# Optimization experiments

Measured on AMD Instinct MI355X. Metric: run time of the kernel, lower is better.

The kernel has to match this reference:

```python
import jax, jax.numpy as jnp
import numpy as np

B, S, D, H = 2, 2048, 1024, 16
DK = D // H
NEG = -1e9


def setup_inputs() -> dict:
    key = jax.random.key(0)
    ks = jax.random.split(key, 11)
    s = 1.0 / np.sqrt(D)
    inp = {
        "q": jax.random.normal(ks[0], (B, S, D), jnp.float32),
        "k": jax.random.normal(ks[1], (B, S, D), jnp.float32),
        "v": jax.random.normal(ks[2], (B, S, D), jnp.float32),
        "mask": jnp.tril(jnp.ones((S, S), jnp.int32))[None, None],  # [1,1,S,S] causal
        "Wq": jax.random.normal(ks[3], (D, D), jnp.float32) * s,
        "bq": jnp.zeros((D,), jnp.float32),
        "Wk": jax.random.normal(ks[4], (D, D), jnp.float32) * s,
        "bk": jnp.zeros((D,), jnp.float32),
        "Wv": jax.random.normal(ks[5], (D, D), jnp.float32) * s,
        "bv": jnp.zeros((D,), jnp.float32),
        "Wo": jax.random.normal(ks[6], (D, D), jnp.float32) * s,
        "bo": jnp.zeros((D,), jnp.float32),
    }
    return inp


def reference(q, k, v, mask, Wq, bq, Wk, bk, Wv, bv, Wo, bo):
    # projections (torch Linear: x @ W.T + b)
    Q = q @ Wq.T + bq
    K = k @ Wk.T + bk
    V = v @ Wv.T + bv
    # [B,S,D] -> [B,H,S,DK]
    Q = Q.reshape(B, S, H, DK).transpose(0, 2, 1, 3)
    K = K.reshape(B, S, H, DK).transpose(0, 2, 1, 3)
    V = V.reshape(B, S, H, DK).transpose(0, 2, 1, 3)
    scores = jnp.einsum("bhqd,bhkd->bhqk", Q, K) / jnp.sqrt(jnp.float32(DK))
    scores = jnp.where(mask == 0, jnp.float32(NEG), scores)
    attn = jax.nn.softmax(scores, axis=-1)  # dropout p=0.0 -> identity
    x = jnp.einsum("bhqk,bhkd->bhqd", attn, V)
    x = x.transpose(0, 2, 1, 3).reshape(B, S, D)
    return x @ Wo.T + bo
```

## Files before the change

kernel.cpp:

```cpp
#include <hip/hip_runtime.h>
#include <hip/hip_bf16.h>


typedef __bf16 bf16_t;
typedef __bf16 bf16x4 __attribute__((ext_vector_type(4)));
typedef __bf16 bf16x8 __attribute__((ext_vector_type(8)));
typedef float f32x4 __attribute__((ext_vector_type(4)));

#define BB 2
#define SS 2048
#define DD 1024
#define HH 16
#define DKK 64
#define MM 4096

#define NELT ((size_t)BB * SS * DD)
#define WELT ((size_t)DD * DD)

__device__ __align__(16) bf16_t g_ws[7 * NELT + 4 * WELT];

__device__ __forceinline__ void gld16(const bf16_t* g, bf16_t* l) {
    __builtin_amdgcn_global_load_lds(
        (const __attribute__((address_space(1))) void*)g,
        (__attribute__((address_space(3))) void*)l, 16, 0, 0);
}

__global__ __launch_bounds__(256) void cvt7(
    const float* __restrict__ q,  const float* __restrict__ k,  const float* __restrict__ v,
    const float* __restrict__ Wq, const float* __restrict__ Wk, const float* __restrict__ Wv,
    const float* __restrict__ Wo,
    bf16_t* __restrict__ qb, bf16_t* __restrict__ kb, bf16_t* __restrict__ vb,
    bf16_t* __restrict__ Wqb, bf16_t* __restrict__ Wkb, bf16_t* __restrict__ Wvb,
    bf16_t* __restrict__ Wob)
{
    const float* s; bf16_t* d; size_t n;
    switch (blockIdx.y) {
        case 0: s = q;  d = qb;  n = NELT; break;
        case 1: s = k;  d = kb;  n = NELT; break;
        case 2: s = v;  d = vb;  n = NELT; break;
        case 3: s = Wq; d = Wqb; n = WELT; break;
        case 4: s = Wk; d = Wkb; n = WELT; break;
        case 5: s = Wv; d = Wvb; n = WELT; break;
        default: s = Wo; d = Wob; n = WELT; break;
    }
    size_t e = ((size_t)blockIdx.x * 256 + threadIdx.x) * 8;
    if (e >= n) return;
    f32x4 a = *(const f32x4*)(s + e);
    f32x4 b = *(const f32x4*)(s + e + 4);
    bf16x8 o;
    #pragma unroll
    for (int i = 0; i < 4; ++i) { o[i] = (bf16_t)a[i]; o[4 + i] = (bf16_t)b[i]; }
    *(bf16x8*)(d + e) = o;
}

#define BM 128
#define BN 128
#define BKG 64
#define LDC 136

__global__ __launch_bounds__(256) void gemm_qkv3(
    const bf16_t* __restrict__ qb, const bf16_t* __restrict__ kb, const bf16_t* __restrict__ vb,
    const bf16_t* __restrict__ Wqb, const bf16_t* __restrict__ Wkb, const bf16_t* __restrict__ Wvb,
    const float* __restrict__ bq, const float* __restrict__ bk, const float* __restrict__ bv,
    bf16_t* __restrict__ Qp, bf16_t* __restrict__ Kp, bf16_t* __restrict__ Vt)
{
    const int z = blockIdx.z;
    const bf16_t* A    = (z == 0) ? qb  : (z == 1) ? kb  : vb;
    const bf16_t* W    = (z == 0) ? Wqb : (z == 1) ? Wkb : Wvb;
    const float*  bias = (z == 0) ? bq  : (z == 1) ? bk  : bv;

    __shared__ __align__(16) bf16_t smem[128 * LDC];
    bf16_t (*As)[BKG] = (bf16_t(*)[BKG])smem;
    bf16_t (*Bs)[BKG] = (bf16_t(*)[BKG])(smem + 128 * BKG);
    bf16_t (*Ct)[LDC] = (bf16_t(*)[LDC])smem;

    const int tid  = threadIdx.x;
    const int wave = tid >> 6;
    const int lane = tid & 63;
    const int quad = lane >> 4;
    const int c16  = lane & 15;
    const int bm = blockIdx.x * BM;
    const int bn = blockIdx.y * BN;
    const int wm = (wave >> 1) * 64;
    const int wn = (wave & 1) * 64;

    const int srow = lane >> 3;
    const int scol = (lane & 7) * 8;

    f32x4 acc[4][4] = {};

    for (int k0 = 0; k0 < DD; k0 += BKG) {
        __syncthreads();
        #pragma unroll
        for (int j = 0; j < 4; ++j) {
            int r0 = wave * 32 + j * 8;
            gld16(A + (size_t)(bm + r0 + srow) * DD + k0 + scol, &As[r0][0]);
            gld16(W + (size_t)(bn + r0 + srow) * DD + k0 + scol, &Bs[r0][0]);
        }
        __syncthreads();

        #pragma unroll
        for (int ks = 0; ks < 2; ++ks) {
            bf16x8 af[4], bfr[4];
            #pragma unroll
            for (int tm = 0; tm < 4; ++tm)
                af[tm] = *(const bf16x8*)(&As[wm + tm * 16 + c16][ks * 32 + quad * 8]);
            #pragma unroll
            for (int tn = 0; tn < 4; ++tn)
                bfr[tn] = *(const bf16x8*)(&Bs[wn + tn * 16 + c16][ks * 32 + quad * 8]);
            #pragma unroll
            for (int tm = 0; tm < 4; ++tm)
                #pragma unroll
                for (int tn = 0; tn < 4; ++tn)
                    acc[tm][tn] = __builtin_amdgcn_mfma_f32_16x16x32_bf16(
                        af[tm], bfr[tn], acc[tm][tn], 0, 0, 0);
        }
    }

    float bia[4];
    #pragma unroll
    for (int tn = 0; tn < 4; ++tn)
        bia[tn] = bias[bn + wn + tn * 16 + c16];

    if (z < 2) {
        const float osc = (z == 0) ? 0.125f : 1.0f;
        bf16_t* C = (z == 0) ? Qp : Kp;
        #pragma unroll
        for (int tm = 0; tm < 4; ++tm)
            #pragma unroll
            for (int r = 0; r < 4; ++r) {
                size_t base = (size_t)(bm + wm + tm * 16 + quad * 4 + r) * DD;
                #pragma unroll
                for (int tn = 0; tn < 4; ++tn)
                    C[base + bn + wn + tn * 16 + c16] =
                        (bf16_t)((acc[tm][tn][r] + bia[tn]) * osc);
            }
    } else {
        __syncthreads();
        #pragma unroll
        for (int tm = 0; tm < 4; ++tm)
            #pragma unroll
            for (int tn = 0; tn < 4; ++tn) {
                bf16x4 pk;
                #pragma unroll
                for (int r = 0; r < 4; ++r)
                    pk[r] = (bf16_t)(acc[tm][tn][r] + bia[tn]);
                *(bf16x4*)(&Ct[wn + tn * 16 + c16][wm + tm * 16 + quad * 4]) = pk;
            }
        __syncthreads();
        const int b_    = bm >> 11;
        const int sbase = bm & (SS - 1);
        #pragma unroll
        for (int p = 0; p < 4; ++p) {
            int col = p * 32 + (tid >> 3);
            int si  = (tid & 7) * 8;
            size_t rowoff = (size_t)(b_ * 1024 + bn + col) * SS + sbase;
            #pragma unroll
            for (int half = 0; half < 2; ++half) {
                int s = si + half * 64;
                *(bf16x8*)(&Vt[rowoff + s]) = *(const bf16x8*)(&Ct[col][s]);
            }
        }
    }
}

__global__ __launch_bounds__(256) void gemm_out(
    const bf16_t* __restrict__ A,
    const bf16_t* __restrict__ W,
    const float* __restrict__ bias,
    float* __restrict__ C)
{
    __shared__ __align__(16) bf16_t As[128][BKG];
    __shared__ __align__(16) bf16_t Bs[64][BKG];

    const int tid  = threadIdx.x;
    const int wave = tid >> 6;
    const int lane = tid & 63;
    const int quad = lane >> 4;
    const int c16  = lane & 15;
    const int bm = blockIdx.x * 128;
    const int bn = blockIdx.y * 64;
    const int wm = (wave >> 1) * 64;
    const int wn = (wave & 1) * 32;

    const int srow = lane >> 3;
    const int scol = (lane & 7) * 8;

    f32x4 acc[4][2] = {};

    for (int k0 = 0; k0 < DD; k0 += BKG) {
        __syncthreads();
        #pragma unroll
        for (int j = 0; j < 4; ++j) {
            int r0 = wave * 32 + j * 8;
            gld16(A + (size_t)(bm + r0 + srow) * DD + k0 + scol, &As[r0][0]);
        }
        #pragma unroll
        for (int j = 0; j < 2; ++j) {
            int r0 = wave * 16 + j * 8;
            gld16(W + (size_t)(bn + r0 + srow) * DD + k0 + scol, &Bs[r0][0]);
        }
        __syncthreads();

        #pragma unroll
        for (int ks = 0; ks < 2; ++ks) {
            bf16x8 af[4], bfr[2];
            #pragma unroll
            for (int tm = 0; tm < 4; ++tm)
                af[tm] = *(const bf16x8*)(&As[wm + tm * 16 + c16][ks * 32 + quad * 8]);
            #pragma unroll
            for (int tn = 0; tn < 2; ++tn)
                bfr[tn] = *(const bf16x8*)(&Bs[wn + tn * 16 + c16][ks * 32 + quad * 8]);
            #pragma unroll
            for (int tm = 0; tm < 4; ++tm)
                #pragma unroll
                for (int tn = 0; tn < 2; ++tn)
                    acc[tm][tn] = __builtin_amdgcn_mfma_f32_16x16x32_bf16(
                        af[tm], bfr[tn], acc[tm][tn], 0, 0, 0);
        }
    }

    float bia[2];
    #pragma unroll
    for (int tn = 0; tn < 2; ++tn)
        bia[tn] = bias[bn + wn + tn * 16 + c16];

    #pragma unroll
    for (int tm = 0; tm < 4; ++tm)
        #pragma unroll
        for (int r = 0; r < 4; ++r) {
            size_t base = (size_t)(bm + wm + tm * 16 + quad * 4 + r) * DD;
            #pragma unroll
            for (int tn = 0; tn < 2; ++tn)
                C[base + bn + wn + tn * 16 + c16] = acc[tm][tn][r] + bia[tn];
        }
}

#define LDPS 40
#define LDCF 68

__global__ __launch_bounds__(256) void attn_fwd7(
    const bf16_t* __restrict__ Q,
    const bf16_t* __restrict__ K,
    const bf16_t* __restrict__ Vt,
    bf16_t* __restrict__ O)
{
    const int flat = blockIdx.x;
    const int bh   = (flat & 7) * 4 + (flat >> 8);
    const int pair = (flat >> 3) & 31;
    const int b = bh >> 4;
    const int h = bh & 15;

    const int wave = threadIdx.x >> 6;
    const int lane = threadIdx.x & 63;
    const int quad = lane >> 4;
    const int c16  = lane & 15;

    __shared__ __align__(16) unsigned char smraw[4 * 16 * LDCF * 4];
    bf16_t (*Ps)[32][LDPS] = (bf16_t(*)[32][LDPS])smraw;
    float  (*Cf)[16][LDCF] = (float(*)[16][LDCF])smraw;
    __shared__ float Ls[4][32];

    const bf16_t* Kb = K  + (size_t)b * SS * DD + h * DKK;
    const bf16_t* Vb = Vt + (size_t)(b * 1024 + h * DKK) * SS;

    bf16_t*       pw = &Ps[wave][c16][quad * 4];
    const bf16_t* pr = &Ps[wave][c16][quad * 8];

    for (int t = 0; t < 2; ++t) {
        const int qt    = (t == 0) ? (63 - pair) : pair;
        const int qbase = qt * 32;
        const int U     = qt + 1;
        const int kend  = U * 32;

        bf16x8 qf[2][2];
        #pragma unroll
        for (int tm = 0; tm < 2; ++tm) {
            const bf16_t* qp = Q + ((size_t)b * SS + qbase + tm * 16 + c16) * DD + h * DKK;
            qf[tm][0] = *(const bf16x8*)(qp + quad * 8);
            qf[tm][1] = *(const bf16x8*)(qp + 32 + quad * 8);
        }

        f32x4 oacc[2][4] = {};
        float lsum2[2] = {0.f, 0.f};

        bf16x8 kfA[2][2], kfB[2][2];
        {
            int kb = wave * 32;
            #pragma unroll
            for (int ct = 0; ct < 2; ++ct) {
                const bf16_t* kp = Kb + (size_t)(kb + ct * 16 + c16) * DD;
                kfA[ct][0] = *(const bf16x8*)(kp + quad * 8);
                kfA[ct][1] = *(const bf16x8*)(kp + 32 + quad * 8);
            }
        }

        auto step = [&](int kb, bf16x8 (&kfc)[2][2], bf16x8 (&kfn)[2][2]) {
            f32x4 sc[2][2];
            #pragma unroll
            for (int tm = 0; tm < 2; ++tm)
                #pragma unroll
                for (int ct = 0; ct < 2; ++ct) {
                    f32x4 s = {};
                    s = __builtin_amdgcn_mfma_f32_16x16x32_bf16(kfc[ct][0], qf[tm][0], s, 0, 0, 0);
                    s = __builtin_amdgcn_mfma_f32_16x16x32_bf16(kfc[ct][1], qf[tm][1], s, 0, 0, 0);
                    sc[tm][ct] = s;
                }

            if (kb + 128 < kend) {
                #pragma unroll
                for (int ct = 0; ct < 2; ++ct) {
                    const bf16_t* kp = Kb + (size_t)(kb + 128 + ct * 16 + c16) * DD;
                    kfn[ct][0] = *(const bf16x8*)(kp + quad * 8);
                    kfn[ct][1] = *(const bf16x8*)(kp + 32 + quad * 8);
                }
            }

            bf16x8 vf[4];
            #pragma unroll
            for (int tn = 0; tn < 4; ++tn)
                vf[tn] = *(const bf16x8*)(Vb + (size_t)(tn * 16 + c16) * SS + kb + quad * 8);

            const bool needmask = (kb == qbase);
            #pragma unroll
            for (int tm = 0; tm < 2; ++tm) {
                const int qrow = qbase + tm * 16 + c16;
                #pragma unroll
                for (int ct = 0; ct < 2; ++ct) {
                    bf16x4 w;
                    #pragma unroll
                    for (int r = 0; r < 4; ++r) {
                        float s = sc[tm][ct][r];
                        if (needmask && (kb + ct * 16 + quad * 4 + r > qrow)) s = -1e9f;
                        float p = __expf(s);
                        lsum2[tm] += p;
                        w[r] = (bf16_t)p;
                    }
                    *(bf16x4*)(pw + tm * 16 * LDPS + ct * 16) = w;
                }
            }

            asm volatile("s_waitcnt lgkmcnt(0)" ::: "memory");

            #pragma unroll
            for (int tm = 0; tm < 2; ++tm) {
                bf16x8 pa = *(const bf16x8*)(pr + tm * 16 * LDPS);
                #pragma unroll
                for (int tn = 0; tn < 4; ++tn)
                    oacc[tm][tn] = __builtin_amdgcn_mfma_f32_16x16x32_bf16(
                        pa, vf[tn], oacc[tm][tn], 0, 0, 0);
            }
        };

        {
            int u = wave; bool cur = false;
            while (u < U) {
                if (!cur) step(u * 32, kfA, kfB);
                else      step(u * 32, kfB, kfA);
                u += 4; cur = !cur;
            }
        }

        #pragma unroll
        for (int tm = 0; tm < 2; ++tm) {
            float l = lsum2[tm];
            l += __shfl_xor(l, 16, 64);
            l += __shfl_xor(l, 32, 64);
            if (lane < 16) Ls[wave][tm * 16 + lane] = l;
        }

        const int row = threadIdx.x >> 4;
        const int col = (threadIdx.x & 15) * 4;
        #pragma unroll
        for (int tm = 0; tm < 2; ++tm) {
            __syncthreads();
            #pragma unroll
            for (int tn = 0; tn < 4; ++tn)
                #pragma unroll
                for (int r = 0; r < 4; ++r)
                    Cf[wave][quad * 4 + r][tn * 16 + c16] = oacc[tm][tn][r];
            __syncthreads();
            f32x4 ssum = {};
            #pragma unroll
            for (int p = 0; p < 4; ++p)
                ssum += *(const f32x4*)(&Cf[p][row][col]);
            float l = Ls[0][tm * 16 + row] + Ls[1][tm * 16 + row]
                    + Ls[2][tm * 16 + row] + Ls[3][tm * 16 + row];
            float inv = 1.0f / l;
            bf16x4 o;
            #pragma unroll
            for (int i = 0; i < 4; ++i) o[i] = (bf16_t)(ssum[i] * inv);
            *(bf16x4*)(&O[((size_t)b * SS + qbase + tm * 16 + row) * DD + h * DKK + col]) = o;
        }
        __syncthreads();
    }
}

extern "C" void kernel_launch(void* const* d_in, const int* in_sizes, int n_in,
                              void* d_out, int out_size, void* d_ws, size_t ws_size,
                              hipStream_t stream) {
    (void)in_sizes; (void)n_in; (void)out_size; (void)d_ws; (void)ws_size;
    const float* q  = (const float*)d_in[0];
    const float* k  = (const float*)d_in[1];
    const float* v  = (const float*)d_in[2];
    const float* Wq = (const float*)d_in[4];
    const float* bq = (const float*)d_in[5];
    const float* Wk = (const float*)d_in[6];
    const float* bk = (const float*)d_in[7];
    const float* Wv = (const float*)d_in[8];
    const float* bv = (const float*)d_in[9];
    const float* Wo = (const float*)d_in[10];
    const float* bo = (const float*)d_in[11];

    bf16_t* ws;
    hipGetSymbolAddress((void**)&ws, HIP_SYMBOL(g_ws));
    bf16_t* Qp  = ws;
    bf16_t* Kp  = Qp + NELT;
    bf16_t* Vt  = Kp + NELT;
    bf16_t* Xa  = Vt + NELT;
    bf16_t* qb  = Xa + NELT;
    bf16_t* kb  = qb + NELT;
    bf16_t* vb  = kb + NELT;
    bf16_t* Wqb = vb + NELT;
    bf16_t* Wkb = Wqb + WELT;
    bf16_t* Wvb = Wkb + WELT;
    bf16_t* Wob = Wvb + WELT;

    cvt7<<<dim3(2048, 7), 256, 0, stream>>>(q, k, v, Wq, Wk, Wv, Wo,
                                            qb, kb, vb, Wqb, Wkb, Wvb, Wob);

    gemm_qkv3<<<dim3(MM / BM, DD / BN, 3), 256, 0, stream>>>(
        qb, kb, vb, Wqb, Wkb, Wvb, bq, bk, bv, Qp, Kp, Vt);

    attn_fwd7<<<dim3(1024), 256, 0, stream>>>(Qp, Kp, Vt, Xa);

    gemm_out<<<dim3(MM / 128, DD / 64), 256, 0, stream>>>(Xa, Wob, bo, (float*)d_out);
}
```

Measured before the change: 276.3 us.

## Software-pipeline attention: overlap PV of previous tile with QK/softmax of current

Restructures the attention inner loop so each step computes QK scores and exp for the current key tile while issuing the P·V MFMAs for the previous tile, using double-buffered LDS slots for P and double-buffered V fragments. This removes the explicit lgkmcnt wait between the P store and the P reload within the same step, letting LDS latency hide behind independent work. LDS usage doubles for the P buffer and register pressure rises from the extra V fragment set, which may reduce occupancy.

```diff
diff --git a/kernel.cpp b/kernel.cpp
--- a/kernel.cpp
+++ b/kernel.cpp
@@ -238,8 +238,86 @@
 
 #define LDPS 40
 #define LDCF 68
-
-__global__ __launch_bounds__(256) void attn_fwd7(
+#define PSLOT (4 * 32 * LDPS)
+
+#define LOADK(KF, UU)                                                          \
+do {                                                                           \
+    const int kb_ = (UU) * 32;                                                 \
+    const bf16_t* kp0 = Kb + (size_t)(kb_ + c16) * DD;                         \
+    const bf16_t* kp1 = Kb + (size_t)(kb_ + 16 + c16) * DD;                    \
+    KF[0][0] = *(const bf16x8*)(kp0 + quad * 8);                               \
+    KF[0][1] = *(const bf16x8*)(kp0 + 32 + quad * 8);                          \
+    KF[1][0] = *(const bf16x8*)(kp1 + quad * 8);                               \
+    KF[1][1] = *(const bf16x8*)(kp1 + 32 + quad * 8);                          \
+} while (0)
+
+#define ATTN_STEP(UU, KFC, KFN, VFC, VFP, PW, PR, DOPV)                        \
+do {                                                                           \
+    const int kb_ = (UU) * 32;                                                 \
+    f32x4 sc_[2][2];                                                           \
+    _Pragma("unroll")                                                          \
+    for (int tm = 0; tm < 2; ++tm)                                             \
+        _Pragma("unroll")                                                      \
+        for (int ct = 0; ct < 2; ++ct) {                                       \
+            f32x4 s_ = {};                                                     \
+            s_ = __builtin_amdgcn_mfma_f32_16x16x32_bf16(                      \
+                     KFC[ct][0], qf[tm][0], s_, 0, 0, 0);                      \
+            s_ = __builtin_amdgcn_mfma_f32_16x16x32_bf16(                      \
+                     KFC[ct][1], qf[tm][1], s_, 0, 0, 0);                      \
+            sc_[tm][ct] = s_;                                                  \
+        }                                                                      \
+    if ((UU) + 4 < U) LOADK(KFN, (UU) + 4);                                    \
+    _Pragma("unroll")                                                          \
+    for (int tn = 0; tn < 4; ++tn)                                             \
+        VFC[tn] = *(const bf16x8*)(Vb + (size_t)(tn * 16 + c16) * SS           \
+                                   + kb_ + quad * 8);                          \
+    const bool needmask_ = (kb_ == qbase);                                     \
+    bf16x4 w_[2][2];                                                           \
+    _Pragma("unroll")                                                          \
+    for (int tm = 0; tm < 2; ++tm) {                                           \
+        const int qrow_ = qbase + tm * 16 + c16;                               \
+        _Pragma("unroll")                                                      \
+        for (int ct = 0; ct < 2; ++ct)                                         \
+            _Pragma("unroll")                                                  \
+            for (int r = 0; r < 4; ++r) {                                      \
+                float s_ = sc_[tm][ct][r];                                     \
+                if (needmask_ && (kb_ + ct * 16 + quad * 4 + r > qrow_))       \
+                    s_ = -1e9f;                                                \
+                float p_ = __expf(s_);                                         \
+                lsum2[tm] += p_;                                               \
+                w_[tm][ct][r] = (bf16_t)p_;                                    \
+            }                                                                  \
+    }                                                                          \
+    if (DOPV) {                                                                \
+        _Pragma("unroll")                                                      \
+        for (int tm = 0; tm < 2; ++tm) {                                       \
+            bf16x8 pa_ = *(const bf16x8*)((PR) + tm * 16 * LDPS);              \
+            _Pragma("unroll")                                                  \
+            for (int tn = 0; tn < 4; ++tn)                                     \
+                oacc[tm][tn] = __builtin_amdgcn_mfma_f32_16x16x32_bf16(        \
+                    pa_, VFP[tn], oacc[tm][tn], 0, 0, 0);                      \
+        }                                                                      \
+    }                                                                          \
+    _Pragma("unroll")                                                          \
+    for (int tm = 0; tm < 2; ++tm)                                             \
+        _Pragma("unroll")                                                      \
+        for (int ct = 0; ct < 2; ++ct)                                         \
+            *(bf16x4*)((PW) + tm * 16 * LDPS + ct * 16) = w_[tm][ct];          \
+} while (0)
+
+#define PVFIN(PR, VFP)                                                         \
+do {                                                                           \
+    _Pragma("unroll")                                                          \
+    for (int tm = 0; tm < 2; ++tm) {                                           \
+        bf16x8 pa_ = *(const bf16x8*)((PR) + tm * 16 * LDPS);                  \
+        _Pragma("unroll")                                                      \
+        for (int tn = 0; tn < 4; ++tn)                                         \
+            oacc[tm][tn] = __builtin_amdgcn_mfma_f32_16x16x32_bf16(            \
+                pa_, VFP[tn], oacc[tm][tn], 0, 0, 0);                          \
+    }                                                                          \
+} while (0)
+
+__global__ __launch_bounds__(256) void attn_fwd9(
     const bf16_t* __restrict__ Q,
     const bf16_t* __restrict__ K,
     const bf16_t* __restrict__ Vt,
@@ -256,22 +334,23 @@
     const int quad = lane >> 4;
     const int c16  = lane & 15;
 
-    __shared__ __align__(16) unsigned char smraw[4 * 16 * LDCF * 4];
-    bf16_t (*Ps)[32][LDPS] = (bf16_t(*)[32][LDPS])smraw;
-    float  (*Cf)[16][LDCF] = (float(*)[16][LDCF])smraw;
+    __shared__ __align__(16) unsigned char smraw[2 * PSLOT * 2];
+    bf16_t (*Ps)[4][32][LDPS] = (bf16_t(*)[4][32][LDPS])smraw;
+    float  (*Cf)[16][LDCF]    = (float(*)[16][LDCF])smraw;
     __shared__ float Ls[4][32];
 
     const bf16_t* Kb = K  + (size_t)b * SS * DD + h * DKK;
     const bf16_t* Vb = Vt + (size_t)(b * 1024 + h * DKK) * SS;
 
-    bf16_t*       pw = &Ps[wave][c16][quad * 4];
-    const bf16_t* pr = &Ps[wave][c16][quad * 8];
+    bf16_t*       pw0 = &Ps[0][wave][c16][quad * 4];
+    const bf16_t* pr0 = &Ps[0][wave][c16][quad * 8];
+    bf16_t*       pw1 = pw0 + PSLOT;
+    const bf16_t* pr1 = pr0 + PSLOT;
 
     for (int t = 0; t < 2; ++t) {
         const int qt    = (t == 0) ? (63 - pair) : pair;
         const int qbase = qt * 32;
         const int U     = qt + 1;
-        const int kend  = U * 32;
 
         bf16x8 qf[2][2];
         #pragma unroll
@@ -285,79 +364,22 @@
         float lsum2[2] = {0.f, 0.f};
 
         bf16x8 kfA[2][2], kfB[2][2];
+        bf16x8 vfA[4], vfB[4];
+
         {
-            int kb = wave * 32;
-            #pragma unroll
-            for (int ct = 0; ct < 2; ++ct) {
-                const bf16_t* kp = Kb + (size_t)(kb + ct * 16 + c16) * DD;
-                kfA[ct][0] = *(const bf16x8*)(kp + quad * 8);
-                kfA[ct][1] = *(const bf16x8*)(kp + 32 + quad * 8);
-            }
-        }
-
-        auto step = [&](int kb, bf16x8 (&kfc)[2][2], bf16x8 (&kfn)[2][2]) {
-            f32x4 sc[2][2];
-            #pragma unroll
-            for (int tm = 0; tm < 2; ++tm)
-                #pragma unroll
-                for (int ct = 0; ct < 2; ++ct) {
-                    f32x4 s = {};
-                    s = __builtin_amdgcn_mfma_f32_16x16x32_bf16(kfc[ct][0], qf[tm][0], s, 0, 0, 0);
-                    s = __builtin_amdgcn_mfma_f32_16x16x32_bf16(kfc[ct][1], qf[tm][1], s, 0, 0, 0);
-                    sc[tm][ct] = s;
+            int u = wave;
+            if (u < U) {
+                LOADK(kfA, u);
+                ATTN_STEP(u, kfA, kfB, vfA, vfB, pw0, pr1, 0);
+                u += 4;
+                for (;;) {
+                    if (u >= U) { PVFIN(pr0, vfA); break; }
+                    ATTN_STEP(u, kfB, kfA, vfB, vfA, pw1, pr0, 1);
+                    u += 4;
+                    if (u >= U) { PVFIN(pr1, vfB); break; }
+                    ATTN_STEP(u, kfA, kfB, vfA, vfB, pw0, pr1, 1);
+                    u += 4;
                 }
-
-            if (kb + 128 < kend) {
-                #pragma unroll
-                for (int ct = 0; ct < 2; ++ct) {
-                    const bf16_t* kp = Kb + (size_t)(kb + 128 + ct * 16 + c16) * DD;
-                    kfn[ct][0] = *(const bf16x8*)(kp + quad * 8);
-                    kfn[ct][1] = *(const bf16x8*)(kp + 32 + quad * 8);
-                }
-            }
-
-            bf16x8 vf[4];
-            #pragma unroll
-            for (int tn = 0; tn < 4; ++tn)
-                vf[tn] = *(const bf16x8*)(Vb + (size_t)(tn * 16 + c16) * SS + kb + quad * 8);
-
-            const bool needmask = (kb == qbase);
-            #pragma unroll
-            for (int tm = 0; tm < 2; ++tm) {
-                const int qrow = qbase + tm * 16 + c16;
-                #pragma unroll
-                for (int ct = 0; ct < 2; ++ct) {
-                    bf16x4 w;
-                    #pragma unroll
-                    for (int r = 0; r < 4; ++r) {
-                        float s = sc[tm][ct][r];
-                        if (needmask && (kb + ct * 16 + quad * 4 + r > qrow)) s = -1e9f;
-                        float p = __expf(s);
-                        lsum2[tm] += p;
-                        w[r] = (bf16_t)p;
-                    }
-                    *(bf16x4*)(pw + tm * 16 * LDPS + ct * 16) = w;
-                }
-            }
-
-            asm volatile("s_waitcnt lgkmcnt(0)" ::: "memory");
-
-            #pragma unroll
-            for (int tm = 0; tm < 2; ++tm) {
-                bf16x8 pa = *(const bf16x8*)(pr + tm * 16 * LDPS);
-                #pragma unroll
-                for (int tn = 0; tn < 4; ++tn)
-                    oacc[tm][tn] = __builtin_amdgcn_mfma_f32_16x16x32_bf16(
-                        pa, vf[tn], oacc[tm][tn], 0, 0, 0);
-            }
-        };
-
-        {
-            int u = wave; bool cur = false;
-            while (u < U) {
-                if (!cur) step(u * 32, kfA, kfB);
-                else      step(u * 32, kfB, kfA);
-                u += 4; cur = !cur;
             }
         }
 
@@ -432,7 +454,7 @@
     gemm_qkv3<<<dim3(MM / BM, DD / BN, 3), 256, 0, stream>>>(
         qb, kb, vb, Wqb, Wkb, Wvb, bq, bk, bv, Qp, Kp, Vt);
 
-    attn_fwd7<<<dim3(1024), 256, 0, stream>>>(Qp, Kp, Vt, Xa);
+    attn_fwd9<<<dim3(1024), 256, 0, stream>>>(Qp, Kp, Vt, Xa);
 
     gemm_out<<<dim3(MM / 128, DD / 64), 256, 0, stream>>>(Xa, Wob, bo, (float*)d_out);
 }
```

Result: slower. 285.6 us (+3.4%).
